# Optimization experiments

Hardware: AMD Instinct MI355X
Metric: run time of the kernel (lower is better)

The kernel has to match this reference:

```python
import jax, jax.numpy as jnp
import numpy as np
from jax import lax

B, L, V, E, F, C, K = 8, 2500, 50000, 100, 50, 8921, 10
PAD = K // 2  # padding=floor(filter_size/2) -> output length L+1 for even K


def setup_inputs() -> dict:
    key = jax.random.key(0)
    ks = jax.random.split(key, 7)
    text = jax.random.randint(ks[0], (B, L), 0, V, dtype=jnp.int32)
    embed_weight = jax.random.normal(ks[1], (V, E), jnp.float32) * 0.1
    embed_weight = embed_weight.at[0].set(0.0)  # padding_idx=0
    conv_w = jax.random.normal(ks[2], (F, E, K), jnp.float32) * (2.0 / (E * K + F)) ** 0.5
    conv_b = jnp.zeros((F,), jnp.float32)
    Q_w = jax.random.normal(ks[3], (C, F), jnp.float32) * (2.0 / (C + F)) ** 0.5
    out_w = jax.random.normal(ks[4], (C, F), jnp.float32) * (2.0 / (C + F)) ** 0.5
    out_b = jnp.zeros((C,), jnp.float32)
    return {"text": text, "embed_weight": embed_weight, "conv_w": conv_w,
            "conv_b": conv_b, "Q_w": Q_w, "out_w": out_w, "out_b": out_b}


def reference(text, embed_weight, conv_w, conv_b, Q_w, out_w, out_b):
    # Embedding lookup (dropout omitted: eval mode): (B, L, E)
    x = embed_weight[text]
    # Conv1d over length: torch Conv1d(E, F, K, padding=PAD)
    x = jnp.transpose(x, (0, 2, 1))  # (B, E, L)
    z = lax.conv_general_dilated(x, conv_w, window_strides=(1,),
                                 padding=[(PAD, PAD)],
                                 dimension_numbers=("NCH", "OIH", "NCH"))
    z = z + conv_b[None, :, None]
    Z = jnp.tanh(jnp.transpose(z, (0, 2, 1)))  # (B, L', F), L' = L+1
    # Per-label attention: Q_w (C,F) @ Z^T -> (B, C, L'), softmax over length
    scores = jnp.einsum("cf,blf->bcl", Q_w, Z)
    alpha = jax.nn.softmax(scores, axis=2)  # (B, C, L')
    # Attention-weighted sum: (B, C, F)
    Ecf = jnp.einsum("bcl,blf->bcf", alpha, Z)
    # Per-class dot-product readout
    logits = jnp.sum(out_w[None] * Ecf, axis=2) + out_b  # (B, C)
    return logits, alpha
```

## Files before the change

### kernel.cpp

```cpp
#include <hip/hip_runtime.h>
#include <math.h>

#define BB 8
#define LL 2500
#define VV 50000
#define EE 100
#define FF 50
#define CC 8921
#define KK 10
#define PADW 5
#define LOUT 2501
#define NLT 157
#define LPAD (NLT * 16)
#define NCT 140
#define NT16 (NCT * 4)

typedef __attribute__((ext_vector_type(8))) short bf16x8;
typedef __attribute__((ext_vector_type(4))) float f32x4;

__device__ __forceinline__ short to_bf16(float f) {
  unsigned u = __builtin_bit_cast(unsigned, f);
  u += 0x7FFFu + ((u >> 16) & 1u);
  return (short)(u >> 16);
}

__global__ void k1_conv(const int* __restrict__ text,
                        const float* __restrict__ embed,
                        const float* __restrict__ convw,
                        const float* __restrict__ convb,
                        short* __restrict__ Z16) {
  __shared__ float xw[73 * 101];
  const int b   = blockIdx.y;
  const int l0  = blockIdx.x * 64;
  const int tid = threadIdx.x;

  for (int idx = tid; idx < 73 * 100; idx += 256) {
    int r = idx / 100;
    int e = idx - r * 100;
    int t = l0 - PADW + r;
    float v = 0.f;
    if (t >= 0 && t < LL) {
      int tok = text[b * LL + t];
      v = embed[tok * EE + e];
    }
    xw[r * 101 + e] = v;
  }
  __syncthreads();

  const int ll = tid & 63;
  const int fg = __builtin_amdgcn_readfirstlane(tid >> 6);
  const int l  = l0 + ll;

  float acc[13];
#pragma unroll
  for (int j = 0; j < 13; ++j) {
    int f = fg + 4 * j;
    acc[j] = (f < FF) ? convb[f] : 0.f;
  }

  for (int e = 0; e < EE; ++e) {
    float xk[KK];
#pragma unroll
    for (int k = 0; k < KK; ++k) xk[k] = xw[(ll + k) * 101 + e];
#pragma unroll
    for (int j = 0; j < 13; ++j) {
      int f = fg + 4 * j;
      if (f < FF) {
        const float* wp = convw + (f * EE + e) * KK;
#pragma unroll
        for (int k = 0; k < KK; ++k) acc[j] += xk[k] * wp[k];
      }
    }
  }

  if (l < LPAD) {
#pragma unroll
    for (int j = 0; j < 13; ++j) {
      int f = fg + 4 * j;
      if (f < FF) {
        float v = (l < LOUT) ? tanhf(acc[j]) : 0.f;
        Z16[((size_t)b * LPAD + l) * 64 + f] = to_bf16(v);
      }
    }
  }
  for (int idx = tid; idx < 64 * 14; idx += 256) {
    int r = idx / 14, k = 50 + idx % 14;
    int lz = l0 + r;
    if (lz < LPAD) Z16[((size_t)b * LPAD + lz) * 64 + k] = 0;
  }
}

__global__ void k_packW(const float* __restrict__ W, short* __restrict__ Wp) {
  int u = blockIdx.x * 256 + threadIdx.x;
  int lane = u & 63, kh = (u >> 6) & 1, t16 = u >> 7;
  int c  = t16 * 16 + (lane & 15);
  int k0 = 4 * (lane >> 4) + 32 * kh;
  union { short s[8]; uint4 v; } o;
#pragma unroll
  for (int j = 0; j < 8; ++j) {
    int k = k0 + (j & 3) + 16 * (j >> 2);
    float val = (c < CC && k < FF) ? W[c * FF + k] : 0.f;
    o.s[j] = to_bf16(val);
  }
  ((uint4*)Wp)[u] = o.v;
}

__global__ void k_packZ(const short* __restrict__ Z16, short* __restrict__ Zp) {
  int u = blockIdx.x * 256 + threadIdx.x;
  int lane = u & 63, kh = (u >> 6) & 1, t = u >> 7;
  int lt = t % NLT, b = t / NLT;
  int l  = lt * 16 + (lane & 15);
  int k0 = 4 * (lane >> 4) + 32 * kh;
  const short* src = Z16 + ((size_t)b * LPAD + l) * 64 + k0;
  uint2 a  = *(const uint2*)src;
  uint2 bb = *(const uint2*)(src + 16);
  uint4 o; o.x = a.x; o.y = a.y; o.z = bb.x; o.w = bb.y;
  ((uint4*)Zp)[u] = o;
}

__global__ __launch_bounds__(256) void k_attn(
    const short* __restrict__ Zp, const short* __restrict__ Qp,
    const short* __restrict__ Op, const float* __restrict__ outb,
    float* __restrict__ alpha, float* __restrict__ logits) {
  const int b    = blockIdx.y;
  const int ct   = blockIdx.x;
  const int tid  = threadIdx.x;
  const int w    = tid >> 6;
  const int lane = tid & 63;
  const int g    = lane >> 4, col = lane & 15;
  const int cb   = ct * 64;

  bf16x8 qf[4][2], of[4][2];
#pragma unroll
  for (int mf = 0; mf < 4; ++mf)
#pragma unroll
    for (int kh = 0; kh < 2; ++kh) {
      int t16 = ct * 4 + mf;
      qf[mf][kh] = ((const bf16x8*)Qp)[(t16 * 2 + kh) * 64 + lane];
      of[mf][kh] = ((const bf16x8*)Op)[(t16 * 2 + kh) * 64 + lane];
    }
  const bf16x8* Zb = (const bf16x8*)Zp + (size_t)b * NLT * 2 * 64;

  float dacc[4][4];
#pragma unroll
  for (int mf = 0; mf < 4; ++mf)
#pragma unroll
    for (int r = 0; r < 4; ++r) dacc[mf][r] = 0.f;

  for (int lt = w; lt < NLT; lt += 4) {
    bf16x8 z0 = Zb[(lt * 2 + 0) * 64 + lane];
    bf16x8 z1 = Zb[(lt * 2 + 1) * 64 + lane];
    int   l    = lt * 16 + col;
    float lmsk = (l < LOUT) ? 1.f : 0.f;
#pragma unroll
    for (int mf = 0; mf < 4; ++mf) {
      f32x4 acc = {0.f, 0.f, 0.f, 0.f};
      acc = __builtin_amdgcn_mfma_f32_16x16x32_bf16(qf[mf][0], z0, acc, 0, 0, 0);
      acc = __builtin_amdgcn_mfma_f32_16x16x32_bf16(qf[mf][1], z1, acc, 0, 0, 0);
#pragma unroll
      for (int r = 0; r < 4; ++r) dacc[mf][r] += lmsk * __expf(acc[r]);
    }
  }

  __shared__ float red[4][4][4][4];
  __shared__ float rdinv[64];
#pragma unroll
  for (int mf = 0; mf < 4; ++mf)
#pragma unroll
    for (int r = 0; r < 4; ++r) {
      float v = dacc[mf][r];
      v += __shfl_xor(v, 1); v += __shfl_xor(v, 2);
      v += __shfl_xor(v, 4); v += __shfl_xor(v, 8);
      dacc[mf][r] = v;
    }
  if (col == 0)
#pragma unroll
    for (int mf = 0; mf < 4; ++mf)
#pragma unroll
      for (int r = 0; r < 4; ++r) red[w][mf][g][r] = dacc[mf][r];
  __syncthreads();
  if (tid < 64) {
    int mf = tid >> 4, gg = (tid >> 2) & 3, r = tid & 3;
    float s = red[0][mf][gg][r] + red[1][mf][gg][r] +
              red[2][mf][gg][r] + red[3][mf][gg][r];
    rdinv[tid] = 1.f / s;
  }
  __syncthreads();

  float rd[4][4];
#pragma unroll
  for (int mf = 0; mf < 4; ++mf)
#pragma unroll
    for (int r = 0; r < 4; ++r) rd[mf][r] = rdinv[mf * 16 + g * 4 + r];

  float lacc[4][4];
#pragma unroll
  for (int mf = 0; mf < 4; ++mf)
#pragma unroll
    for (int r = 0; r < 4; ++r) lacc[mf][r] = 0.f;

  for (int lt = w; lt < NLT; lt += 4) {
    bf16x8 z0 = Zb[(lt * 2 + 0) * 64 + lane];
    bf16x8 z1 = Zb[(lt * 2 + 1) * 64 + lane];
    int  l    = lt * 16 + col;
    bool lval = (l < LOUT);
#pragma unroll
    for (int mf = 0; mf < 4; ++mf) {
      f32x4 s = {0.f, 0.f, 0.f, 0.f}, t = {0.f, 0.f, 0.f, 0.f};
      s = __builtin_amdgcn_mfma_f32_16x16x32_bf16(qf[mf][0], z0, s, 0, 0, 0);
      s = __builtin_amdgcn_mfma_f32_16x16x32_bf16(qf[mf][1], z1, s, 0, 0, 0);
      t = __builtin_amdgcn_mfma_f32_16x16x32_bf16(of[mf][0], z0, t, 0, 0, 0);
      t = __builtin_amdgcn_mfma_f32_16x16x32_bf16(of[mf][1], z1, t, 0, 0, 0);
#pragma unroll
      for (int r = 0; r < 4; ++r) {
        float a = __expf(s[r]) * rd[mf][r];
        int   c = cb + mf * 16 + g * 4 + r;
        if (lval && c < CC)
          alpha[(size_t)(b * CC + c) * LOUT + l] = a;
        lacc[mf][r] += lval ? a * t[r] : 0.f;
      }
    }
  }

#pragma unroll
  for (int mf = 0; mf < 4; ++mf)
#pragma unroll
    for (int r = 0; r < 4; ++r) {
      float v = lacc[mf][r];
      v += __shfl_xor(v, 1); v += __shfl_xor(v, 2);
      v += __shfl_xor(v, 4); v += __shfl_xor(v, 8);
      lacc[mf][r] = v;
    }
  if (col == 0)
#pragma unroll
    for (int mf = 0; mf < 4; ++mf)
#pragma unroll
      for (int r = 0; r < 4; ++r) red[w][mf][g][r] = lacc[mf][r];
  __syncthreads();
  if (tid < 64) {
    int mf = tid >> 4, gg = (tid >> 2) & 3, r = tid & 3;
    int c = cb + tid;
    if (c < CC) {
      float v = red[0][mf][gg][r] + red[1][mf][gg][r] +
                red[2][mf][gg][r] + red[3][mf][gg][r];
      logits[b * CC + c] = v + outb[c];
    }
  }
}

extern "C" void kernel_launch(void* const* d_in, const int* in_sizes, int n_in,
                              void* d_out, int out_size, void* d_ws, size_t ws_size,
                              hipStream_t stream) {
  const int*   text  = (const int*)d_in[0];
  const float* embed = (const float*)d_in[1];
  const float* convw = (const float*)d_in[2];
  const float* convb = (const float*)d_in[3];
  const float* Qw    = (const float*)d_in[4];
  const float* outw  = (const float*)d_in[5];
  const float* outb  = (const float*)d_in[6];

  float* out    = (float*)d_out;
  float* logits = out;
  float* alpha  = out + (size_t)BB * CC;

  short* Z16 = (short*)alpha;

  short* wsS = (short*)d_ws;
  short* Zp  = wsS;
  short* Qp  = Zp + (size_t)BB * NLT * 2 * 64 * 8;
  short* Op  = Qp + (size_t)NT16 * 2 * 64 * 8;

  k1_conv<<<dim3((LPAD + 63) / 64, BB), 256, 0, stream>>>(
      text, embed, convw, convb, Z16);
  k_packW<<<(NT16 * 128) / 256, 256, 0, stream>>>(Qw, Qp);
  k_packW<<<(NT16 * 128) / 256, 256, 0, stream>>>(outw, Op);
  k_packZ<<<(BB * NLT * 128) / 256, 256, 0, stream>>>(Z16, Zp);
  k_attn<<<dim3(NCT, BB), 256, 0, stream>>>(Zp, Qp, Op, outb, alpha, logits);
}
```

Baseline: 681.1 us.

## Stage alpha tiles in LDS for coalesced 64-wide row stores and batch Z loads

The attention kernel now processes four contiguous L-tiles per wave per step, loading their Z fragments together. Alpha values are staged through a per-wave LDS tile so each 16-class row is written as 64 contiguous floats, replacing the scattered 16-wide strided global stores. The grid is flattened with batch as the fastest index, so blocks sharing a class tile run close together and reuse Q/O weights in cache. The cost is extra LDS traffic, more registers for the batched fragments, and an added barrier before the final reduction.

```diff
diff --git a/kernel.cpp b/kernel.cpp
--- a/kernel.cpp
+++ b/kernel.cpp
@@ -14,6 +14,7 @@
 #define LPAD (NLT * 16)
 #define NCT 140
 #define NT16 (NCT * 4)
+#define NG 10
 
 typedef __attribute__((ext_vector_type(8))) short bf16x8;
 typedef __attribute__((ext_vector_type(4))) float f32x4;
@@ -122,14 +123,19 @@
     const short* __restrict__ Zp, const short* __restrict__ Qp,
     const short* __restrict__ Op, const float* __restrict__ outb,
     float* __restrict__ alpha, float* __restrict__ logits) {
-  const int b    = blockIdx.y;
-  const int ct   = blockIdx.x;
+  const int id   = blockIdx.x;
+  const int b    = id & 7;
+  const int ct   = id >> 3;
   const int tid  = threadIdx.x;
   const int w    = tid >> 6;
   const int lane = tid & 63;
   const int g    = lane >> 4, col = lane & 15;
   const int cb   = ct * 64;
 
+  __shared__ float red[4][4][4][4];
+  __shared__ float rdinv[64];
+  __shared__ float sA[4 * 16 * 68];
+
   bf16x8 qf[4][2], of[4][2];
 #pragma unroll
   for (int mf = 0; mf < 4; ++mf)
@@ -147,23 +153,30 @@
 #pragma unroll
     for (int r = 0; r < 4; ++r) dacc[mf][r] = 0.f;
 
-  for (int lt = w; lt < NLT; lt += 4) {
-    bf16x8 z0 = Zb[(lt * 2 + 0) * 64 + lane];
-    bf16x8 z1 = Zb[(lt * 2 + 1) * 64 + lane];
-    int   l    = lt * 16 + col;
-    float lmsk = (l < LOUT) ? 1.f : 0.f;
-#pragma unroll
-    for (int mf = 0; mf < 4; ++mf) {
-      f32x4 acc = {0.f, 0.f, 0.f, 0.f};
-      acc = __builtin_amdgcn_mfma_f32_16x16x32_bf16(qf[mf][0], z0, acc, 0, 0, 0);
-      acc = __builtin_amdgcn_mfma_f32_16x16x32_bf16(qf[mf][1], z1, acc, 0, 0, 0);
-#pragma unroll
-      for (int r = 0; r < 4; ++r) dacc[mf][r] += lmsk * __expf(acc[r]);
-    }
-  }
-
-  __shared__ float red[4][4][4][4];
-  __shared__ float rdinv[64];
+  for (int t = 0; t < NG; ++t) {
+    const int lt0 = t * 16 + w * 4;
+    bf16x8 zz[4][2];
+#pragma unroll
+    for (int i = 0; i < 4; ++i) {
+      int lt = lt0 + i; if (lt > NLT - 1) lt = NLT - 1;
+      zz[i][0] = Zb[(lt * 2 + 0) * 64 + lane];
+      zz[i][1] = Zb[(lt * 2 + 1) * 64 + lane];
+    }
+#pragma unroll
+    for (int i = 0; i < 4; ++i) {
+      int   l    = (lt0 + i) * 16 + col;
+      float lmsk = (l < LOUT) ? 1.f : 0.f;
+#pragma unroll
+      for (int mf = 0; mf < 4; ++mf) {
+        f32x4 acc = {0.f, 0.f, 0.f, 0.f};
+        acc = __builtin_amdgcn_mfma_f32_16x16x32_bf16(qf[mf][0], zz[i][0], acc, 0, 0, 0);
+        acc = __builtin_amdgcn_mfma_f32_16x16x32_bf16(qf[mf][1], zz[i][1], acc, 0, 0, 0);
+#pragma unroll
+        for (int r = 0; r < 4; ++r) dacc[mf][r] += lmsk * __expf(acc[r]);
+      }
+    }
+  }
+
 #pragma unroll
   for (int mf = 0; mf < 4; ++mf)
 #pragma unroll
@@ -199,25 +212,41 @@
 #pragma unroll
     for (int r = 0; r < 4; ++r) lacc[mf][r] = 0.f;
 
-  for (int lt = w; lt < NLT; lt += 4) {
-    bf16x8 z0 = Zb[(lt * 2 + 0) * 64 + lane];
-    bf16x8 z1 = Zb[(lt * 2 + 1) * 64 + lane];
-    int  l    = lt * 16 + col;
-    bool lval = (l < LOUT);
+  float* sAw = sA + w * (16 * 68);
+
+  for (int t = 0; t < NG; ++t) {
+    const int lt0 = t * 16 + w * 4;
+    bf16x8 zz[4][2];
+#pragma unroll
+    for (int i = 0; i < 4; ++i) {
+      int lt = lt0 + i; if (lt > NLT - 1) lt = NLT - 1;
+      zz[i][0] = Zb[(lt * 2 + 0) * 64 + lane];
+      zz[i][1] = Zb[(lt * 2 + 1) * 64 + lane];
+    }
 #pragma unroll
     for (int mf = 0; mf < 4; ++mf) {
-      f32x4 s = {0.f, 0.f, 0.f, 0.f}, t = {0.f, 0.f, 0.f, 0.f};
-      s = __builtin_amdgcn_mfma_f32_16x16x32_bf16(qf[mf][0], z0, s, 0, 0, 0);
-      s = __builtin_amdgcn_mfma_f32_16x16x32_bf16(qf[mf][1], z1, s, 0, 0, 0);
-      t = __builtin_amdgcn_mfma_f32_16x16x32_bf16(of[mf][0], z0, t, 0, 0, 0);
-      t = __builtin_amdgcn_mfma_f32_16x16x32_bf16(of[mf][1], z1, t, 0, 0, 0);
-#pragma unroll
-      for (int r = 0; r < 4; ++r) {
-        float a = __expf(s[r]) * rd[mf][r];
-        int   c = cb + mf * 16 + g * 4 + r;
-        if (lval && c < CC)
-          alpha[(size_t)(b * CC + c) * LOUT + l] = a;
-        lacc[mf][r] += lval ? a * t[r] : 0.f;
+#pragma unroll
+      for (int i = 0; i < 4; ++i) {
+        f32x4 s = {0.f, 0.f, 0.f, 0.f}, tt = {0.f, 0.f, 0.f, 0.f};
+        s  = __builtin_amdgcn_mfma_f32_16x16x32_bf16(qf[mf][0], zz[i][0], s, 0, 0, 0);
+        s  = __builtin_amdgcn_mfma_f32_16x16x32_bf16(qf[mf][1], zz[i][1], s, 0, 0, 0);
+        tt = __builtin_amdgcn_mfma_f32_16x16x32_bf16(of[mf][0], zz[i][0], tt, 0, 0, 0);
+        tt = __builtin_amdgcn_mfma_f32_16x16x32_bf16(of[mf][1], zz[i][1], tt, 0, 0, 0);
+        int l = (lt0 + i) * 16 + col;
+#pragma unroll
+        for (int r = 0; r < 4; ++r) {
+          float a = __expf(s[r]) * rd[mf][r];
+          lacc[mf][r] += (l < LOUT) ? a * tt[r] : 0.f;
+          sAw[(g * 4 + r) * 68 + i * 16 + col] = a;
+        }
+      }
+      const int l0w = lt0 * 16;
+      const int lw  = l0w + lane;
+#pragma unroll
+      for (int rr = 0; rr < 16; ++rr) {
+        int c = cb + mf * 16 + rr;
+        if (lw < LOUT && c < CC)
+          alpha[(size_t)(b * CC + c) * LOUT + lw] = sAw[rr * 68 + lane];
       }
     }
   }
@@ -231,6 +260,7 @@
       v += __shfl_xor(v, 4); v += __shfl_xor(v, 8);
       lacc[mf][r] = v;
     }
+  __syncthreads();
   if (col == 0)
 #pragma unroll
     for (int mf = 0; mf < 4; ++mf)
@@ -275,5 +305,5 @@
   k_packW<<<(NT16 * 128) / 256, 256, 0, stream>>>(Qw, Qp);
   k_packW<<<(NT16 * 128) / 256, 256, 0, stream>>>(outw, Op);
   k_packZ<<<(BB * NLT * 128) / 256, 256, 0, stream>>>(Z16, Zp);
-  k_attn<<<dim3(NCT, BB), 256, 0, stream>>>(Zp, Qp, Op, outb, alpha, logits);
-}
+  k_attn<<<dim3(NCT * BB), 256, 0, stream>>>(Zp, Qp, Op, outb, alpha, logits);
+}
```

Result: no change. 693.8 us (+1.9%).

## Restructure attention kernel: per-wave class rows, LDS-staged coalesced alpha stores

Applied to the files above, without the earlier changes.

Each wave now owns one 16-class tile and walks the full sequence, so softmax denominators are reduced within the wave and no block-level barriers are needed. Alpha values are staged in shared memory in 256-column chunks and written back as contiguous float4 rows instead of scattered scalar stores along the class dimension. Z tiles are software-prefetched one step ahead, and the grid is flattened so consecutive blocks interleave batches and share the same Q/O tiles. In exchange the kernel uses about 66KB of LDS per block, which lowers occupancy, and each wave runs a longer serial loop.

```diff
diff --git a/kernel.cpp b/kernel.cpp
--- a/kernel.cpp
+++ b/kernel.cpp
@@ -14,6 +14,7 @@
 #define LPAD (NLT * 16)
 #define NCT 140
 #define NT16 (NCT * 4)
+#define SROW 260
 
 typedef __attribute__((ext_vector_type(8))) short bf16x8;
 typedef __attribute__((ext_vector_type(4))) float f32x4;
@@ -122,128 +123,115 @@
     const short* __restrict__ Zp, const short* __restrict__ Qp,
     const short* __restrict__ Op, const float* __restrict__ outb,
     float* __restrict__ alpha, float* __restrict__ logits) {
-  const int b    = blockIdx.y;
-  const int ct   = blockIdx.x;
+  const int id   = blockIdx.x;
+  const int b    = id & 7;
+  const int ct   = id >> 3;
   const int tid  = threadIdx.x;
   const int w    = tid >> 6;
   const int lane = tid & 63;
   const int g    = lane >> 4, col = lane & 15;
-  const int cb   = ct * 64;
-
-  bf16x8 qf[4][2], of[4][2];
-#pragma unroll
-  for (int mf = 0; mf < 4; ++mf)
-#pragma unroll
-    for (int kh = 0; kh < 2; ++kh) {
-      int t16 = ct * 4 + mf;
-      qf[mf][kh] = ((const bf16x8*)Qp)[(t16 * 2 + kh) * 64 + lane];
-      of[mf][kh] = ((const bf16x8*)Op)[(t16 * 2 + kh) * 64 + lane];
-    }
+  const int crow = ct * 64 + w * 16;
+
+  __shared__ float sA[4 * 16 * SROW];
+  float* sAw = sA + w * (16 * SROW);
+
+  bf16x8 qf0, qf1, of0, of1;
+  {
+    int t16 = ct * 4 + w;
+    qf0 = ((const bf16x8*)Qp)[(t16 * 2 + 0) * 64 + lane];
+    qf1 = ((const bf16x8*)Qp)[(t16 * 2 + 1) * 64 + lane];
+    of0 = ((const bf16x8*)Op)[(t16 * 2 + 0) * 64 + lane];
+    of1 = ((const bf16x8*)Op)[(t16 * 2 + 1) * 64 + lane];
+  }
   const bf16x8* Zb = (const bf16x8*)Zp + (size_t)b * NLT * 2 * 64;
 
-  float dacc[4][4];
-#pragma unroll
-  for (int mf = 0; mf < 4; ++mf)
-#pragma unroll
-    for (int r = 0; r < 4; ++r) dacc[mf][r] = 0.f;
-
-  for (int lt = w; lt < NLT; lt += 4) {
-    bf16x8 z0 = Zb[(lt * 2 + 0) * 64 + lane];
-    bf16x8 z1 = Zb[(lt * 2 + 1) * 64 + lane];
-    int   l    = lt * 16 + col;
-    float lmsk = (l < LOUT) ? 1.f : 0.f;
-#pragma unroll
-    for (int mf = 0; mf < 4; ++mf) {
-      f32x4 acc = {0.f, 0.f, 0.f, 0.f};
-      acc = __builtin_amdgcn_mfma_f32_16x16x32_bf16(qf[mf][0], z0, acc, 0, 0, 0);
-      acc = __builtin_amdgcn_mfma_f32_16x16x32_bf16(qf[mf][1], z1, acc, 0, 0, 0);
-#pragma unroll
-      for (int r = 0; r < 4; ++r) dacc[mf][r] += lmsk * __expf(acc[r]);
-    }
-  }
-
-  __shared__ float red[4][4][4][4];
-  __shared__ float rdinv[64];
-#pragma unroll
-  for (int mf = 0; mf < 4; ++mf)
+  float dacc[4] = {0.f, 0.f, 0.f, 0.f};
+  {
+    bf16x8 zc0, zc1, zn0, zn1;
+    zn0 = Zb[0 * 64 + lane];
+    zn1 = Zb[1 * 64 + lane];
+    for (int lt = 0; lt < NLT; ++lt) {
+      zc0 = zn0; zc1 = zn1;
+      if (lt + 1 < NLT) {
+        zn0 = Zb[((lt + 1) * 2 + 0) * 64 + lane];
+        zn1 = Zb[((lt + 1) * 2 + 1) * 64 + lane];
+      }
+      const int   l    = lt * 16 + col;
+      const float lmsk = (l < LOUT) ? 1.f : 0.f;
+      f32x4 s = {0.f, 0.f, 0.f, 0.f};
+      s = __builtin_amdgcn_mfma_f32_16x16x32_bf16(qf0, zc0, s, 0, 0, 0);
+      s = __builtin_amdgcn_mfma_f32_16x16x32_bf16(qf1, zc1, s, 0, 0, 0);
+#pragma unroll
+      for (int r = 0; r < 4; ++r) dacc[r] += lmsk * __expf(s[r]);
+    }
+  }
+  float rd[4];
+#pragma unroll
+  for (int r = 0; r < 4; ++r) {
+    float v = dacc[r];
+    v += __shfl_xor(v, 1); v += __shfl_xor(v, 2);
+    v += __shfl_xor(v, 4); v += __shfl_xor(v, 8);
+    rd[r] = 1.f / v;
+  }
+
+  float lacc[4] = {0.f, 0.f, 0.f, 0.f};
+  {
+    bf16x8 zc0, zc1, zn0, zn1;
+    zn0 = Zb[0 * 64 + lane];
+    zn1 = Zb[1 * 64 + lane];
+    for (int lt = 0; lt < NLT; ++lt) {
+      zc0 = zn0; zc1 = zn1;
+      if (lt + 1 < NLT) {
+        zn0 = Zb[((lt + 1) * 2 + 0) * 64 + lane];
+        zn1 = Zb[((lt + 1) * 2 + 1) * 64 + lane];
+      }
+      f32x4 s = {0.f, 0.f, 0.f, 0.f}, tt = {0.f, 0.f, 0.f, 0.f};
+      s  = __builtin_amdgcn_mfma_f32_16x16x32_bf16(qf0, zc0, s, 0, 0, 0);
+      s  = __builtin_amdgcn_mfma_f32_16x16x32_bf16(qf1, zc1, s, 0, 0, 0);
+      tt = __builtin_amdgcn_mfma_f32_16x16x32_bf16(of0, zc0, tt, 0, 0, 0);
+      tt = __builtin_amdgcn_mfma_f32_16x16x32_bf16(of1, zc1, tt, 0, 0, 0);
+      const int l = lt * 16 + col;
+#pragma unroll
+      for (int r = 0; r < 4; ++r) {
+        float a = __expf(s[r]) * rd[r];
+        lacc[r] += (l < LOUT) ? a * tt[r] : 0.f;
+        sAw[(g * 4 + r) * SROW + (lt & 15) * 16 + col] = a;
+      }
+      if ((lt & 15) == 15 || lt == NLT - 1) {
+        const int l0  = (lt & ~15) * 16;
+        int rem = LOUT - l0; if (rem > 256) rem = 256;
+        const int i4 = 4 * lane;
+#pragma unroll 4
+        for (int rr = 0; rr < 16; ++rr) {
+          int c = crow + rr;
+          if (c < CC) {
+            float* dst = alpha + (size_t)((size_t)b * CC + c) * LOUT + l0;
+            const float* src = sAw + rr * SROW;
+            if (i4 + 4 <= rem) {
+              *(float4*)(dst + i4) = *(const float4*)(src + i4);
+            } else if (i4 < rem) {
+#pragma unroll
+              for (int j = 0; j < 4; ++j)
+                if (i4 + j < rem) dst[i4 + j] = src[i4 + j];
+            }
+          }
+        }
+      }
+    }
+  }
+
+#pragma unroll
+  for (int r = 0; r < 4; ++r) {
+    float v = lacc[r];
+    v += __shfl_xor(v, 1); v += __shfl_xor(v, 2);
+    v += __shfl_xor(v, 4); v += __shfl_xor(v, 8);
+    lacc[r] = v;
+  }
+  if (col == 0) {
 #pragma unroll
     for (int r = 0; r < 4; ++r) {
-      float v = dacc[mf][r];
-      v += __shfl_xor(v, 1); v += __shfl_xor(v, 2);
-      v += __shfl_xor(v, 4); v += __shfl_xor(v, 8);
-      dacc[mf][r] = v;
-    }
-  if (col == 0)
-#pragma unroll
-    for (int mf = 0; mf < 4; ++mf)
-#pragma unroll
-      for (int r = 0; r < 4; ++r) red[w][mf][g][r] = dacc[mf][r];
-  __syncthreads();
-  if (tid < 64) {
-    int mf = tid >> 4, gg = (tid >> 2) & 3, r = tid & 3;
-    float s = red[0][mf][gg][r] + red[1][mf][gg][r] +
-              red[2][mf][gg][r] + red[3][mf][gg][r];
-    rdinv[tid] = 1.f / s;
-  }
-  __syncthreads();
-
-  float rd[4][4];
-#pragma unroll
-  for (int mf = 0; mf < 4; ++mf)
-#pragma unroll
-    for (int r = 0; r < 4; ++r) rd[mf][r] = rdinv[mf * 16 + g * 4 + r];
-
-  float lacc[4][4];
-#pragma unroll
-  for (int mf = 0; mf < 4; ++mf)
-#pragma unroll
-    for (int r = 0; r < 4; ++r) lacc[mf][r] = 0.f;
-
-  for (int lt = w; lt < NLT; lt += 4) {
-    bf16x8 z0 = Zb[(lt * 2 + 0) * 64 + lane];
-    bf16x8 z1 = Zb[(lt * 2 + 1) * 64 + lane];
-    int  l    = lt * 16 + col;
-    bool lval = (l < LOUT);
-#pragma unroll
-    for (int mf = 0; mf < 4; ++mf) {
-      f32x4 s = {0.f, 0.f, 0.f, 0.f}, t = {0.f, 0.f, 0.f, 0.f};
-      s = __builtin_amdgcn_mfma_f32_16x16x32_bf16(qf[mf][0], z0, s, 0, 0, 0);
-      s = __builtin_amdgcn_mfma_f32_16x16x32_bf16(qf[mf][1], z1, s, 0, 0, 0);
-      t = __builtin_amdgcn_mfma_f32_16x16x32_bf16(of[mf][0], z0, t, 0, 0, 0);
-      t = __builtin_amdgcn_mfma_f32_16x16x32_bf16(of[mf][1], z1, t, 0, 0, 0);
-#pragma unroll
-      for (int r = 0; r < 4; ++r) {
-        float a = __expf(s[r]) * rd[mf][r];
-        int   c = cb + mf * 16 + g * 4 + r;
-        if (lval && c < CC)
-          alpha[(size_t)(b * CC + c) * LOUT + l] = a;
-        lacc[mf][r] += lval ? a * t[r] : 0.f;
-      }
-    }
-  }
-
-#pragma unroll
-  for (int mf = 0; mf < 4; ++mf)
-#pragma unroll
-    for (int r = 0; r < 4; ++r) {
-      float v = lacc[mf][r];
-      v += __shfl_xor(v, 1); v += __shfl_xor(v, 2);
-      v += __shfl_xor(v, 4); v += __shfl_xor(v, 8);
-      lacc[mf][r] = v;
-    }
-  if (col == 0)
-#pragma unroll
-    for (int mf = 0; mf < 4; ++mf)
-#pragma unroll
-      for (int r = 0; r < 4; ++r) red[w][mf][g][r] = lacc[mf][r];
-  __syncthreads();
-  if (tid < 64) {
-    int mf = tid >> 4, gg = (tid >> 2) & 3, r = tid & 3;
-    int c = cb + tid;
-    if (c < CC) {
-      float v = red[0][mf][gg][r] + red[1][mf][gg][r] +
-                red[2][mf][gg][r] + red[3][mf][gg][r];
-      logits[b * CC + c] = v + outb[c];
+      int c = crow + g * 4 + r;
+      if (c < CC) logits[b * CC + c] = lacc[r] + outb[c];
     }
   }
 }
@@ -275,5 +263,5 @@
   k_packW<<<(NT16 * 128) / 256, 256, 0, stream>>>(Qw, Qp);
   k_packW<<<(NT16 * 128) / 256, 256, 0, stream>>>(outw, Op);
   k_packZ<<<(BB * NLT * 128) / 256, 256, 0, stream>>>(Z16, Zp);
-  k_attn<<<dim3(NCT, BB), 256, 0, stream>>>(Zp, Qp, Op, outb, alpha, logits);
-}
+  k_attn<<<dim3(NCT * BB), 256, 0, stream>>>(Zp, Qp, Op, outb, alpha, logits);
+}
```

Result: slower. 715.6 us (+5.1%).
